# Performance work log

Hardware: AMD Instinct MI355X
Metric: run time of the kernel (lower is better)

## Reference

```python
import jax, jax.numpy as jnp
import numpy as np

WH, WW = 7, 7
N = WH * WW
C = 192
H = 6
D = C // H


def _rel_position_index(Wh, Ww):
    # double_step_seq(2*Ww-1, Wh, 1, Ww)
    seq1 = np.arange(0, (2 * Ww - 1) * Wh, 2 * Ww - 1)
    seq2 = np.arange(0, Ww, 1)
    coords = (seq1[:, None] + seq2[None, :]).reshape(1, -1)  # [1, Wh*Ww]
    idx = coords + coords.T                                   # [N, N]
    idx = idx[:, ::-1].copy()                                 # flip(1)
    return idx

REL_IDX = _rel_position_index(WH, WW)  # static int index [N, N]


def setup_inputs() -> dict:
    key = jax.random.key(0)
    ks = jax.random.split(key, 8)
    B = 8192
    nW = 64
    q = jax.random.normal(ks[0], (B, N, C), dtype=jnp.float32)
    kv = jax.random.normal(ks[1], (B, N, C), dtype=jnp.float32)
    mask = jnp.zeros((nW, N, N), dtype=jnp.float32)
    s = 0.02
    Wq = jax.random.normal(ks[2], (C, C), dtype=jnp.float32) * s
    bq = jnp.zeros((C,), dtype=jnp.float32)
    Wkv = jax.random.normal(ks[3], (2 * C, C), dtype=jnp.float32) * s
    bkv = jnp.zeros((2 * C,), dtype=jnp.float32)
    Wo = jax.random.normal(ks[4], (C, C), dtype=jnp.float32) * s
    bo = jnp.zeros((C,), dtype=jnp.float32)
    rpb_table = jax.random.normal(ks[5], ((2 * WH - 1) * (2 * WW - 1), H), dtype=jnp.float32) * s
    return {"q": q, "kv": kv, "mask": mask, "Wq": Wq, "bq": bq,
            "Wkv": Wkv, "bkv": bkv, "Wo": Wo, "bo": bo, "rpb_table": rpb_table}


def reference(q, kv, mask, Wq, bq, Wkv, bkv, Wo, bo, rpb_table):
    B, Nq, _ = q.shape
    Nk = kv.shape[1]
    scale = D ** -0.5
    qh = (q @ Wq.T + bq).reshape(B, Nq, H, D).transpose(0, 2, 1, 3)  # [B,H,Nq,D]
    kvh = (kv @ Wkv.T + bkv).reshape(B, Nk, 2, H, D)
    kh = kvh[:, :, 0].transpose(0, 2, 1, 3)  # [B,H,Nk,D]
    vh = kvh[:, :, 1].transpose(0, 2, 1, 3)
    attn = jnp.einsum('bhqd,bhkd->bhqk', qh * scale, kh)
    bias = rpb_table[REL_IDX.reshape(-1)].reshape(N, N, H).transpose(2, 0, 1)  # [H,N,N]
    attn = attn + bias[None]
    nW = mask.shape[0]
    attn = attn.reshape(B // nW, nW, H, Nq, Nk) + mask[None, :, None]
    attn = attn.reshape(B, H, Nq, Nk)
    attn = jax.nn.softmax(attn, axis=-1)
    x = jnp.einsum('bhqk,bhkd->bhqd', attn, vh).transpose(0, 2, 1, 3).reshape(B, Nq, C)
    return x @ Wo.T + bo
```

## Files before the change

kernel.cpp:

```cpp
#include <hip/hip_runtime.h>

#define NTOK 49
#define CDIM 192
#define NHEAD 6
#define HDIM 32

typedef float f32x4 __attribute__((ext_vector_type(4), may_alias));
typedef float f32x4u __attribute__((ext_vector_type(4), may_alias, aligned(4)));
typedef short b16x8 __attribute__((ext_vector_type(8), may_alias));
typedef short b16x4 __attribute__((ext_vector_type(4), may_alias));

__device__ __forceinline__ f32x4 MFMA(b16x8 a, b16x8 b, f32x4 c) {
  return __builtin_amdgcn_mfma_f32_16x16x32_bf16(a, b, c, 0, 0, 0);
}

__device__ __forceinline__ short f2bf(float f) {
  unsigned u = __builtin_bit_cast(unsigned, f);
  u += 0x7FFFu + ((u >> 16) & 1u);
  return (short)(u >> 16);
}

__device__ __forceinline__ int swz(int r, int c) {
  return r * 192 + (c ^ ((r & 7) << 3));
}
__device__ __forceinline__ int swz64(int r, int c) {
  return r * 64 + (c ^ ((r & 7) << 3));
}
__device__ __forceinline__ int ps(int r, int c) {
  return r * 32 + (c ^ ((((r & 3) ^ ((r >> 2) & 3)) & 3) << 3));
}

__global__ void prep_w(const float* __restrict__ Wq, const float* __restrict__ Wkv,
                       const float* __restrict__ Wo, short* __restrict__ wsW) {
  const float scale = 0.17677669529663687f;
  int i = blockIdx.x * 256 + threadIdx.x;
  if (i >= 147456) return;
  float v;
  if (i < 36864)        v = Wq[i] * scale;
  else if (i < 110592)  v = Wkv[i - 36864];
  else                  v = Wo[i - 110592];
  wsW[i] = f2bf(v);
}

__global__ void prep_bias(const float* __restrict__ rpb, float* __restrict__ bias_t) {
  int idx = blockIdx.x * 256 + threadIdx.x;
  if (idx >= NHEAD * NTOK * 64) return;
  int k = idx & 63;
  int q = (idx >> 6) % NTOK;
  int h = idx / (NTOK * 64);
  float v = -1e9f;
  if (k < NTOK) {
    int ci = (q / 7) * 13 + (q % 7);
    int jj = 48 - k;
    int cj = (jj / 7) * 13 + (jj % 7);
    v = rpb[(ci + cj) * NHEAD + h];
  }
  bias_t[idx] = v;
}

__global__ __launch_bounds__(512, 4) void wmsa_kernel(
    const float* __restrict__ qg, const float* __restrict__ kvg,
    const float* __restrict__ maskg, const float* __restrict__ bq,
    const float* __restrict__ bkv, const float* __restrict__ bo,
    const short* __restrict__ wsW, const float* __restrict__ bias_t,
    float* __restrict__ outg, int nW) {
  __shared__ short lds[20480];
  short* X = lds;
  short* KH2 = lds + 12288;
  short* VT2 = lds + 16384;
  float* BF = (float*)lds;

  const int b = blockIdx.x;
  const int tid = threadIdx.x;
  const int w = tid >> 6;
  const int lane = tid & 63;
  const int l15 = lane & 15;
  const int lg = lane >> 4;
  const int R = w >> 1, hw = w & 1;
  const f32x4 zero4 = {0.f, 0.f, 0.f, 0.f};

  const short* WqB = wsW;
  const short* WkvB = wsW + 36864;
  const short* WoB = wsW + 110592;

  const float* qsrc = qg + (size_t)b * (NTOK * CDIM);
  const float* kvsrc = kvg + (size_t)b * (NTOK * CDIM);
  const float* maskw = maskg + (size_t)(b % nW) * (NTOK * NTOK);

  const int qrow = R * 16 + l15;
  const int qc = qrow > 48 ? 48 : qrow;

  b16x8 aq6[6];
#pragma unroll
  for (int kk = 0; kk < 6; ++kk) {
    f32x4 lo = *(const f32x4*)(qsrc + qc * CDIM + kk * 32 + lg * 8);
    f32x4 hi = *(const f32x4*)(qsrc + qc * CDIM + kk * 32 + lg * 8 + 4);
    b16x8 a = {f2bf(lo[0]), f2bf(lo[1]), f2bf(lo[2]), f2bf(lo[3]),
               f2bf(hi[0]), f2bf(hi[1]), f2bf(hi[2]), f2bf(hi[3])};
    aq6[kk] = a;
  }
#pragma unroll
  for (int t = 0; t < 6; ++t) {
    const int col = (2 * (t >> 1) + hw) * 32 + (t & 1) * 16 + l15;
    f32x4 acc = zero4;
#pragma unroll
    for (int kk = 0; kk < 6; ++kk) {
      b16x8 bw = *(const b16x8*)(WqB + col * CDIM + kk * 32 + lg * 8);
      acc = MFMA(aq6[kk], bw, acc);
    }
    const float bias = bq[col] * 0.17677669529663687f;
#pragma unroll
    for (int rr = 0; rr < 4; ++rr)
      X[swz(R * 16 + lg * 4 + rr, hw * 96 + t * 16 + l15)] = f2bf(acc[rr] + bias);
  }
  b16x8 aq[3];
#pragma unroll
  for (int p = 0; p < 3; ++p)
    aq[p] = *(const b16x8*)(X + swz(R * 16 + l15, hw * 96 + p * 32 + lg * 8));
  __syncthreads();

#pragma unroll
  for (int it = 0; it < 6; ++it) {
    int idx = tid + it * 512;
    int r = idx / 48, c4 = idx % 48;
    f32x4 v = (r < NTOK) ? *(const f32x4*)(kvsrc + r * CDIM + c4 * 4) : zero4;
    b16x4 o = {f2bf(v[0]), f2bf(v[1]), f2bf(v[2]), f2bf(v[3])};
    *(b16x4*)(X + swz(r, c4 * 4)) = o;
  }
  __syncthreads();

  b16x8 xbf[3];
#pragma unroll
  for (int p = 0; p < 3; ++p) {
    const int ct = w & 3;
    const int isV = w >> 2;
    const int colg = isV * CDIM + p * 64 + ct * 16 + l15;
    f32x4 acc[4];
#pragma unroll
    for (int m = 0; m < 4; ++m) acc[m] = zero4;
#pragma unroll
    for (int kk = 0; kk < 6; ++kk) {
      b16x8 bw = *(const b16x8*)(WkvB + colg * CDIM + kk * 32 + lg * 8);
#pragma unroll
      for (int m = 0; m < 4; ++m) {
        b16x8 a = *(const b16x8*)(X + swz(m * 16 + l15, kk * 32 + lg * 8));
        acc[m] = MFMA(a, bw, acc[m]);
      }
    }
    const float bias = bkv[colg];
    if (!isV) {
#pragma unroll
      for (int m = 0; m < 4; ++m)
#pragma unroll
        for (int rr = 0; rr < 4; ++rr)
          KH2[swz64(m * 16 + lg * 4 + rr, ct * 16 + l15)] = f2bf(acc[m][rr] + bias);
    } else {
#pragma unroll
      for (int m = 0; m < 4; ++m) {
        b16x4 o = {f2bf(acc[m][0] + bias), f2bf(acc[m][1] + bias),
                   f2bf(acc[m][2] + bias), f2bf(acc[m][3] + bias)};
        *(b16x4*)(VT2 + swz64(ct * 16 + l15, m * 16 + lg * 4)) = o;
      }
    }
    __syncthreads();

    const int h = 2 * p + hw;
    f32x4 Ls[4];
#pragma unroll
    for (int nt = 0; nt < 4; ++nt) {
      b16x8 bk = *(const b16x8*)(KH2 + swz64(nt * 16 + l15, hw * 32 + lg * 8));
      Ls[nt] = MFMA(bk, aq[p], zero4);
    }
    const float* bt = bias_t + (h * NTOK + qc) * 64;
#pragma unroll
    for (int nt = 0; nt < 4; ++nt) {
      f32x4 bb = *(const f32x4*)(bt + nt * 16 + lg * 4);
#pragma unroll
      for (int rr = 0; rr < 4; ++rr) Ls[nt][rr] += bb[rr];
    }
#pragma unroll
    for (int nt = 0; nt < 3; ++nt) {
      f32x4 mm = *(const f32x4u*)(maskw + qc * NTOK + nt * 16 + lg * 4);
#pragma unroll
      for (int rr = 0; rr < 4; ++rr) Ls[nt][rr] += mm[rr];
    }
    if (lg == 0) Ls[3][0] += maskw[qc * NTOK + 48];

    float mx = Ls[0][0];
#pragma unroll
    for (int nt = 0; nt < 4; ++nt)
#pragma unroll
      for (int rr = 0; rr < 4; ++rr) mx = fmaxf(mx, Ls[nt][rr]);
    mx = fmaxf(mx, __shfl_xor(mx, 16));
    mx = fmaxf(mx, __shfl_xor(mx, 32));
    float sum = 0.f;
#pragma unroll
    for (int nt = 0; nt < 4; ++nt)
#pragma unroll
      for (int rr = 0; rr < 4; ++rr) {
        Ls[nt][rr] = __expf(Ls[nt][rr] - mx);
        sum += Ls[nt][rr];
      }
    sum += __shfl_xor(sum, 16);
    sum += __shfl_xor(sum, 32);
    const float inv = 1.f / sum;
    __syncthreads();

    short* Pscr = KH2 + w * 512;
    b16x8 ap[2];
#pragma unroll
    for (int kkh = 0; kkh < 2; ++kkh) {
#pragma unroll
      for (int nth = 0; nth < 2; ++nth) {
        const int nt = 2 * kkh + nth;
        b16x4 o = {f2bf(Ls[nt][0] * inv), f2bf(Ls[nt][1] * inv),
                   f2bf(Ls[nt][2] * inv), f2bf(Ls[nt][3] * inv)};
        *(b16x4*)(Pscr + ps(l15, nth * 16 + lg * 4)) = o;
      }
      ap[kkh] = *(const b16x8*)(Pscr + ps(l15, lg * 8));
    }
    f32x4 xa[2] = {zero4, zero4};
#pragma unroll
    for (int kkh = 0; kkh < 2; ++kkh)
#pragma unroll
      for (int nv = 0; nv < 2; ++nv) {
        b16x8 bv = *(const b16x8*)(VT2 + swz64(hw * 32 + nv * 16 + l15, kkh * 32 + lg * 8));
        xa[nv] = MFMA(ap[kkh], bv, xa[nv]);
      }
    b16x8 xb = {f2bf(xa[0][0]), f2bf(xa[0][1]), f2bf(xa[0][2]), f2bf(xa[0][3]),
                f2bf(xa[1][0]), f2bf(xa[1][1]), f2bf(xa[1][2]), f2bf(xa[1][3])};
    xbf[p] = xb;
    __syncthreads();
  }

#pragma unroll
  for (int p = 0; p < 3; ++p) {
    const int h = 2 * p + hw;
#pragma unroll
    for (int nv = 0; nv < 2; ++nv)
#pragma unroll
      for (int rr = 0; rr < 4; ++rr)
        X[swz(R * 16 + lg * 4 + rr, h * 32 + nv * 16 + l15)] = xbf[p][nv * 4 + rr];
  }
  __syncthreads();

  f32x4 oacc[6];
#pragma unroll
  for (int t = 0; t < 6; ++t) oacc[t] = zero4;
#pragma unroll
  for (int t = 0; t < 6; ++t) {
    const int j = 2 * t + (w >> 2);
    const int m = w & 3;
    const int col = j * 16 + l15;
#pragma unroll
    for (int kk = 0; kk < 6; ++kk) {
      b16x8 a = *(const b16x8*)(X + swz(m * 16 + l15, kk * 32 + lg * 8));
      b16x8 bw = *(const b16x8*)(WoB + col * CDIM + kk * 32 + lg * 8);
      oacc[t] = MFMA(a, bw, oacc[t]);
    }
  }
  __syncthreads();

  float* dst = outg + (size_t)b * (NTOK * CDIM);
  if ((w & 3) < 2) {
#pragma unroll
    for (int t = 0; t < 6; ++t) {
      const int col = (2 * t + (w >> 2)) * 16 + l15;
      const float bias = bo[col];
#pragma unroll
      for (int rr = 0; rr < 4; ++rr)
        BF[((w & 3) * 16 + lg * 4 + rr) * 196 + col] = oacc[t][rr] + bias;
    }
  }
  __syncthreads();
#pragma unroll
  for (int it = 0; it < 3; ++it) {
    int idx = tid + it * 512;
    int row = idx / 48, c4 = idx % 48;
    *(f32x4*)(dst + row * CDIM + c4 * 4) = *(const f32x4*)(BF + row * 196 + c4 * 4);
  }
  __syncthreads();
  if ((w & 3) >= 2) {
#pragma unroll
    for (int t = 0; t < 6; ++t) {
      const int col = (2 * t + (w >> 2)) * 16 + l15;
      const float bias = bo[col];
#pragma unroll
      for (int rr = 0; rr < 4; ++rr)
        BF[(((w & 3) - 2) * 16 + lg * 4 + rr) * 196 + col] = oacc[t][rr] + bias;
    }
  }
  __syncthreads();
#pragma unroll
  for (int it = 0; it < 2; ++it) {
    int idx = tid + it * 512;
    if (idx < 17 * 48) {
      int row2 = idx / 48, c4 = idx % 48;
      *(f32x4*)(dst + (32 + row2) * CDIM + c4 * 4) =
          *(const f32x4*)(BF + row2 * 196 + c4 * 4);
    }
  }
}

extern "C" void kernel_launch(void* const* d_in, const int* in_sizes, int n_in,
                              void* d_out, int out_size, void* d_ws, size_t ws_size,
                              hipStream_t stream) {
  const float* q = (const float*)d_in[0];
  const float* kv = (const float*)d_in[1];
  const float* mask = (const float*)d_in[2];
  const float* Wq = (const float*)d_in[3];
  const float* bq = (const float*)d_in[4];
  const float* Wkv = (const float*)d_in[5];
  const float* bkv = (const float*)d_in[6];
  const float* Wo = (const float*)d_in[7];
  const float* bo = (const float*)d_in[8];
  const float* rpb = (const float*)d_in[9];
  short* wsW = (short*)d_ws;
  float* bias_t = (float*)((char*)d_ws + 294912);

  const int B = in_sizes[0] / (NTOK * CDIM);
  const int nW = in_sizes[2] / (NTOK * NTOK);

  prep_w<<<576, 256, 0, stream>>>(Wq, Wkv, Wo, wsW);
  prep_bias<<<(NHEAD * NTOK * 64 + 255) / 256, 256, 0, stream>>>(rpb, bias_t);
  wmsa_kernel<<<B, 512, 0, stream>>>(q, kv, mask, bq, bkv, bo, wsW, bias_t,
                                     (float*)d_out, nW);
}
```

Before: 965.3 us.

## Split KV projection into separate kernel writing K and transposed V to global memory

Moves the K/V projection out of the per-window attention kernel into a dense row-tiled GEMM kernel that writes bf16 K rows and a transposed V layout to workspace. The attention kernel then reads K and V directly from global memory, which removes the per-head projection loop and several block-wide barriers and shrinks LDS use. The cost is an extra global round trip of the K/V activations. There are also risks: VSTRIDE is hardcoded to the batch size, the V loads index past 49 columns into neighbouring windows, and kproj reads rows past the end when the row count is not a multiple of 64.

After: 1.463 ms. +51.6%, slower.

```diff
diff --git a/kernel.cpp b/kernel.cpp
--- a/kernel.cpp
+++ b/kernel.cpp
@@ -4,6 +4,7 @@
 #define CDIM 192
 #define NHEAD 6
 #define HDIM 32
+#define VSTRIDE 401424
 
 typedef float f32x4 __attribute__((ext_vector_type(4), may_alias));
 typedef float f32x4u __attribute__((ext_vector_type(4), may_alias, aligned(4)));
@@ -22,9 +23,6 @@
 
 __device__ __forceinline__ int swz(int r, int c) {
   return r * 192 + (c ^ ((r & 7) << 3));
-}
-__device__ __forceinline__ int swz64(int r, int c) {
-  return r * 64 + (c ^ ((r & 7) << 3));
 }
 __device__ __forceinline__ int ps(int r, int c) {
   return r * 32 + (c ^ ((((r & 3) ^ ((r >> 2) & 3)) & 3) << 3));
@@ -58,16 +56,93 @@
   bias_t[idx] = v;
 }
 
-__global__ __launch_bounds__(512, 4) void wmsa_kernel(
-    const float* __restrict__ qg, const float* __restrict__ kvg,
-    const float* __restrict__ maskg, const float* __restrict__ bq,
-    const float* __restrict__ bkv, const float* __restrict__ bo,
+__global__ __launch_bounds__(256, 4) void kproj_kernel(
+    const float* __restrict__ kvg, const float* __restrict__ bkv,
+    const short* __restrict__ wsW, short* __restrict__ khg,
+    short* __restrict__ vtg) {
+  __shared__ short KB[4][640];
+  __shared__ short VB[96 * 72];
+
+  const int blk = blockIdx.x;
+  const int tid = threadIdx.x;
+  const int w = tid >> 6;
+  const int lane = tid & 63;
+  const int l15 = lane & 15;
+  const int lg = lane >> 4;
+  const int r0 = blk * 64 + w * 16;
+  const f32x4 zero4 = {0.f, 0.f, 0.f, 0.f};
+  const short* WkvB = wsW + 36864;
+
+  b16x8 kvf[6];
+#pragma unroll
+  for (int kk = 0; kk < 6; ++kk) {
+    const float* src = kvg + (size_t)(r0 + l15) * CDIM + kk * 32 + lg * 8;
+    f32x4 lo = *(const f32x4*)(src);
+    f32x4 hi = *(const f32x4*)(src + 4);
+    b16x8 a = {f2bf(lo[0]), f2bf(lo[1]), f2bf(lo[2]), f2bf(lo[3]),
+               f2bf(hi[0]), f2bf(hi[1]), f2bf(hi[2]), f2bf(hi[3])};
+    kvf[kk] = a;
+  }
+
+#pragma unroll
+  for (int ct = 0; ct < 12; ++ct) {
+    const int col = ct * 16 + l15;
+    f32x4 acc = zero4;
+#pragma unroll
+    for (int kk = 0; kk < 6; ++kk) {
+      b16x8 bw = *(const b16x8*)(WkvB + col * CDIM + kk * 32 + lg * 8);
+      acc = MFMA(kvf[kk], bw, acc);
+    }
+    const float bias = bkv[col];
+#pragma unroll
+    for (int rr = 0; rr < 4; ++rr)
+      KB[w][(lg * 4 + rr) * 40 + (ct & 1) * 16 + l15] = f2bf(acc[rr] + bias);
+    if (ct & 1) {
+      const int row = lane >> 2, seg = lane & 3;
+      b16x8 v = *(const b16x8*)(&KB[w][row * 40 + seg * 8]);
+      *(b16x8*)(khg + (size_t)(r0 + row) * CDIM + (ct - 1) * 16 + seg * 8) = v;
+    }
+  }
+
+#pragma unroll
+  for (int g = 0; g < 2; ++g) {
+#pragma unroll
+    for (int tt = 0; tt < 6; ++tt) {
+      const int col = CDIM + g * 96 + tt * 16 + l15;
+      f32x4 acc = zero4;
+#pragma unroll
+      for (int kk = 0; kk < 6; ++kk) {
+        b16x8 bw = *(const b16x8*)(WkvB + col * CDIM + kk * 32 + lg * 8);
+        acc = MFMA(kvf[kk], bw, acc);
+      }
+      const float bias = bkv[col];
+      b16x4 o = {f2bf(acc[0] + bias), f2bf(acc[1] + bias),
+                 f2bf(acc[2] + bias), f2bf(acc[3] + bias)};
+      *(b16x4*)(&VB[(tt * 16 + l15) * 72 + w * 16 + lg * 4]) = o;
+    }
+    __syncthreads();
+    for (int u = tid; u < 384; u += 256) {
+      const int c = u >> 2, s = u & 2 ? (u & 3) : (u & 3);
+      b16x8 a = *(const b16x8*)(&VB[c * 72 + (u & 3) * 16]);
+      b16x8 b2 = *(const b16x8*)(&VB[c * 72 + (u & 3) * 16 + 8]);
+      short* dst = vtg + (size_t)(g * 96 + c) * VSTRIDE + blk * 64 + (u & 3) * 16;
+      *(b16x8*)(dst) = a;
+      *(b16x8*)(dst + 8) = b2;
+      (void)s;
+    }
+    __syncthreads();
+  }
+}
+
+__global__ __launch_bounds__(512, 4) void attn_kernel(
+    const float* __restrict__ qg, const float* __restrict__ maskg,
+    const float* __restrict__ bq, const float* __restrict__ bo,
     const short* __restrict__ wsW, const float* __restrict__ bias_t,
+    const short* __restrict__ khg, const short* __restrict__ vtg,
     float* __restrict__ outg, int nW) {
-  __shared__ short lds[20480];
+  __shared__ short lds[16384];
   short* X = lds;
-  short* KH2 = lds + 12288;
-  short* VT2 = lds + 16384;
+  short* PS = lds + 12288;
   float* BF = (float*)lds;
 
   const int b = blockIdx.x;
@@ -80,12 +155,11 @@
   const f32x4 zero4 = {0.f, 0.f, 0.f, 0.f};
 
   const short* WqB = wsW;
-  const short* WkvB = wsW + 36864;
   const short* WoB = wsW + 110592;
 
   const float* qsrc = qg + (size_t)b * (NTOK * CDIM);
-  const float* kvsrc = kvg + (size_t)b * (NTOK * CDIM);
   const float* maskw = maskg + (size_t)(b % nW) * (NTOK * NTOK);
+  const short* khb = khg + (size_t)b * 49 * CDIM;
 
   const int qrow = R * 16 + l15;
   const int qc = qrow > 48 ? 48 : qrow;
@@ -119,56 +193,15 @@
     aq[p] = *(const b16x8*)(X + swz(R * 16 + l15, hw * 96 + p * 32 + lg * 8));
   __syncthreads();
 
-#pragma unroll
-  for (int it = 0; it < 6; ++it) {
-    int idx = tid + it * 512;
-    int r = idx / 48, c4 = idx % 48;
-    f32x4 v = (r < NTOK) ? *(const f32x4*)(kvsrc + r * CDIM + c4 * 4) : zero4;
-    b16x4 o = {f2bf(v[0]), f2bf(v[1]), f2bf(v[2]), f2bf(v[3])};
-    *(b16x4*)(X + swz(r, c4 * 4)) = o;
-  }
-  __syncthreads();
-
   b16x8 xbf[3];
 #pragma unroll
   for (int p = 0; p < 3; ++p) {
-    const int ct = w & 3;
-    const int isV = w >> 2;
-    const int colg = isV * CDIM + p * 64 + ct * 16 + l15;
-    f32x4 acc[4];
-#pragma unroll
-    for (int m = 0; m < 4; ++m) acc[m] = zero4;
-#pragma unroll
-    for (int kk = 0; kk < 6; ++kk) {
-      b16x8 bw = *(const b16x8*)(WkvB + colg * CDIM + kk * 32 + lg * 8);
-#pragma unroll
-      for (int m = 0; m < 4; ++m) {
-        b16x8 a = *(const b16x8*)(X + swz(m * 16 + l15, kk * 32 + lg * 8));
-        acc[m] = MFMA(a, bw, acc[m]);
-      }
-    }
-    const float bias = bkv[colg];
-    if (!isV) {
-#pragma unroll
-      for (int m = 0; m < 4; ++m)
-#pragma unroll
-        for (int rr = 0; rr < 4; ++rr)
-          KH2[swz64(m * 16 + lg * 4 + rr, ct * 16 + l15)] = f2bf(acc[m][rr] + bias);
-    } else {
-#pragma unroll
-      for (int m = 0; m < 4; ++m) {
-        b16x4 o = {f2bf(acc[m][0] + bias), f2bf(acc[m][1] + bias),
-                   f2bf(acc[m][2] + bias), f2bf(acc[m][3] + bias)};
-        *(b16x4*)(VT2 + swz64(ct * 16 + l15, m * 16 + lg * 4)) = o;
-      }
-    }
-    __syncthreads();
-
     const int h = 2 * p + hw;
     f32x4 Ls[4];
 #pragma unroll
     for (int nt = 0; nt < 4; ++nt) {
-      b16x8 bk = *(const b16x8*)(KH2 + swz64(nt * 16 + l15, hw * 32 + lg * 8));
+      b16x8 bk = *(const b16x8*)(khb + (size_t)(nt * 16 + l15) * CDIM +
+                                 h * HDIM + lg * 8);
       Ls[nt] = MFMA(bk, aq[p], zero4);
     }
     const float* bt = bias_t + (h * NTOK + qc) * 64;
@@ -204,9 +237,8 @@
     sum += __shfl_xor(sum, 16);
     sum += __shfl_xor(sum, 32);
     const float inv = 1.f / sum;
-    __syncthreads();
-
-    short* Pscr = KH2 + w * 512;
+
+    short* Pscr = PS + w * 512;
     b16x8 ap[2];
 #pragma unroll
     for (int kkh = 0; kkh < 2; ++kkh) {
@@ -224,13 +256,13 @@
     for (int kkh = 0; kkh < 2; ++kkh)
 #pragma unroll
       for (int nv = 0; nv < 2; ++nv) {
-        b16x8 bv = *(const b16x8*)(VT2 + swz64(hw * 32 + nv * 16 + l15, kkh * 32 + lg * 8));
+        b16x8 bv = *(const b16x8*)(vtg + (size_t)(h * HDIM + nv * 16 + l15) * VSTRIDE +
+                                   b * 49 + kkh * 32 + lg * 8);
         xa[nv] = MFMA(ap[kkh], bv, xa[nv]);
       }
     b16x8 xb = {f2bf(xa[0][0]), f2bf(xa[0][1]), f2bf(xa[0][2]), f2bf(xa[0][3]),
                 f2bf(xa[1][0]), f2bf(xa[1][1]), f2bf(xa[1][2]), f2bf(xa[1][3])};
     xbf[p] = xb;
-    __syncthreads();
   }
 
 #pragma unroll
@@ -240,7 +272,7 @@
     for (int nv = 0; nv < 2; ++nv)
 #pragma unroll
       for (int rr = 0; rr < 4; ++rr)
-        X[swz(R * 16 + lg * 4 + rr, h * 32 + nv * 16 + l15)] = xbf[p][nv * 4 + rr];
+        X[swz(R * 16 + lg * 4 + rr, h * HDIM + nv * 16 + l15)] = xbf[p][nv * 4 + rr];
   }
   __syncthreads();
 
@@ -315,14 +347,19 @@
   const float* Wo = (const float*)d_in[7];
   const float* bo = (const float*)d_in[8];
   const float* rpb = (const float*)d_in[9];
+
   short* wsW = (short*)d_ws;
   float* bias_t = (float*)((char*)d_ws + 294912);
+  short* khg = (short*)((char*)d_ws + 370176);
+  short* vtg = khg + (size_t)VSTRIDE * CDIM;
 
   const int B = in_sizes[0] / (NTOK * CDIM);
   const int nW = in_sizes[2] / (NTOK * NTOK);
+  const int nrows = B * NTOK;
 
   prep_w<<<576, 256, 0, stream>>>(Wq, Wkv, Wo, wsW);
   prep_bias<<<(NHEAD * NTOK * 64 + 255) / 256, 256, 0, stream>>>(rpb, bias_t);
-  wmsa_kernel<<<B, 512, 0, stream>>>(q, kv, mask, bq, bkv, bo, wsW, bias_t,
+  kproj_kernel<<<nrows / 64, 256, 0, stream>>>(kv, bkv, wsW, khg, vtg);
+  attn_kernel<<<B, 512, 0, stream>>>(q, mask, bq, bo, wsW, bias_t, khg, vtg,
                                      (float*)d_out, nW);
 }
```

## Compute full K/V projection once and drop per-head-pair barriers

Applied to the files above, without the earlier changes.

The K and V projections for all heads are now computed in a single phase into larger LDS buffers, replacing three interleaved projection and attention rounds. This removes several block-wide barriers per round. The output tile is staged through LDS in one pass instead of two half-passes, and bf16 conversion now uses the compiler's native cast. The cost is LDS growing from about 40KB to 72KB per block, which can cut the number of resident blocks per CU.

Result: slower. 1.243 ms (+28.8%).

```diff
diff --git a/kernel.cpp b/kernel.cpp
--- a/kernel.cpp
+++ b/kernel.cpp
@@ -15,9 +15,8 @@
 }
 
 __device__ __forceinline__ short f2bf(float f) {
-  unsigned u = __builtin_bit_cast(unsigned, f);
-  u += 0x7FFFu + ((u >> 16) & 1u);
-  return (short)(u >> 16);
+  __bf16 h = (__bf16)f;
+  return __builtin_bit_cast(short, h);
 }
 
 __device__ __forceinline__ int swz(int r, int c) {
@@ -64,11 +63,11 @@
     const float* __restrict__ bkv, const float* __restrict__ bo,
     const short* __restrict__ wsW, const float* __restrict__ bias_t,
     float* __restrict__ outg, int nW) {
-  __shared__ short lds[20480];
+  __shared__ short lds[36864];
   short* X = lds;
-  short* KH2 = lds + 12288;
-  short* VT2 = lds + 16384;
-  float* BF = (float*)lds;
+  short* KH = lds + 12288;
+  short* VT = lds + 24576;
+  float* BF = (float*)(lds + 12288);
 
   const int b = blockIdx.x;
   const int tid = threadIdx.x;
@@ -129,46 +128,49 @@
   }
   __syncthreads();
 
-  b16x8 xbf[3];
-#pragma unroll
-  for (int p = 0; p < 3; ++p) {
-    const int ct = w & 3;
-    const int isV = w >> 2;
-    const int colg = isV * CDIM + p * 64 + ct * 16 + l15;
+#pragma unroll
+  for (int jj = 0; jj < 3; ++jj) {
+    const int nt = w * 3 + jj;
+    const int col = nt * 16 + l15;
     f32x4 acc[4];
 #pragma unroll
     for (int m = 0; m < 4; ++m) acc[m] = zero4;
 #pragma unroll
     for (int kk = 0; kk < 6; ++kk) {
-      b16x8 bw = *(const b16x8*)(WkvB + colg * CDIM + kk * 32 + lg * 8);
+      b16x8 bw = *(const b16x8*)(WkvB + col * CDIM + kk * 32 + lg * 8);
 #pragma unroll
       for (int m = 0; m < 4; ++m) {
         b16x8 a = *(const b16x8*)(X + swz(m * 16 + l15, kk * 32 + lg * 8));
         acc[m] = MFMA(a, bw, acc[m]);
       }
     }
-    const float bias = bkv[colg];
-    if (!isV) {
+    const float bias = bkv[col];
+    if (col < CDIM) {
 #pragma unroll
       for (int m = 0; m < 4; ++m)
 #pragma unroll
         for (int rr = 0; rr < 4; ++rr)
-          KH2[swz64(m * 16 + lg * 4 + rr, ct * 16 + l15)] = f2bf(acc[m][rr] + bias);
+          KH[swz(m * 16 + lg * 4 + rr, col)] = f2bf(acc[m][rr] + bias);
     } else {
+      const int c = col - CDIM;
 #pragma unroll
       for (int m = 0; m < 4; ++m) {
         b16x4 o = {f2bf(acc[m][0] + bias), f2bf(acc[m][1] + bias),
                    f2bf(acc[m][2] + bias), f2bf(acc[m][3] + bias)};
-        *(b16x4*)(VT2 + swz64(ct * 16 + l15, m * 16 + lg * 4)) = o;
-      }
-    }
-    __syncthreads();
-
+        *(b16x4*)(VT + swz64(c, m * 16 + lg * 4)) = o;
+      }
+    }
+  }
+  __syncthreads();
+
+  b16x8 xbf[3];
+#pragma unroll
+  for (int p = 0; p < 3; ++p) {
     const int h = 2 * p + hw;
     f32x4 Ls[4];
 #pragma unroll
     for (int nt = 0; nt < 4; ++nt) {
-      b16x8 bk = *(const b16x8*)(KH2 + swz64(nt * 16 + l15, hw * 32 + lg * 8));
+      b16x8 bk = *(const b16x8*)(KH + swz(nt * 16 + l15, h * HDIM + lg * 8));
       Ls[nt] = MFMA(bk, aq[p], zero4);
     }
     const float* bt = bias_t + (h * NTOK + qc) * 64;
@@ -204,9 +206,8 @@
     sum += __shfl_xor(sum, 16);
     sum += __shfl_xor(sum, 32);
     const float inv = 1.f / sum;
-    __syncthreads();
-
-    short* Pscr = KH2 + w * 512;
+
+    short* Pscr = X + w * 512;
     b16x8 ap[2];
 #pragma unroll
     for (int kkh = 0; kkh < 2; ++kkh) {
@@ -224,14 +225,15 @@
     for (int kkh = 0; kkh < 2; ++kkh)
 #pragma unroll
       for (int nv = 0; nv < 2; ++nv) {
-        b16x8 bv = *(const b16x8*)(VT2 + swz64(hw * 32 + nv * 16 + l15, kkh * 32 + lg * 8));
+        b16x8 bv = *(const b16x8*)(VT + swz64(h * HDIM + nv * 16 + l15,
+                                              kkh * 32 + lg * 8));
         xa[nv] = MFMA(ap[kkh], bv, xa[nv]);
       }
     b16x8 xb = {f2bf(xa[0][0]), f2bf(xa[0][1]), f2bf(xa[0][2]), f2bf(xa[0][3]),
                 f2bf(xa[1][0]), f2bf(xa[1][1]), f2bf(xa[1][2]), f2bf(xa[1][3])};
     xbf[p] = xb;
-    __syncthreads();
-  }
+  }
+  __syncthreads();
 
 #pragma unroll
   for (int p = 0; p < 3; ++p) {
@@ -240,7 +242,7 @@
     for (int nv = 0; nv < 2; ++nv)
 #pragma unroll
       for (int rr = 0; rr < 4; ++rr)
-        X[swz(R * 16 + lg * 4 + rr, h * 32 + nv * 16 + l15)] = xbf[p][nv * 4 + rr];
+        X[swz(R * 16 + lg * 4 + rr, h * HDIM + nv * 16 + l15)] = xbf[p][nv * 4 + rr];
   }
   __syncthreads();
 
@@ -261,43 +263,28 @@
   }
   __syncthreads();
 
-  float* dst = outg + (size_t)b * (NTOK * CDIM);
-  if ((w & 3) < 2) {
+  {
+    const int m = w & 3;
 #pragma unroll
     for (int t = 0; t < 6; ++t) {
       const int col = (2 * t + (w >> 2)) * 16 + l15;
       const float bias = bo[col];
 #pragma unroll
-      for (int rr = 0; rr < 4; ++rr)
-        BF[((w & 3) * 16 + lg * 4 + rr) * 196 + col] = oacc[t][rr] + bias;
-    }
-  }
-  __syncthreads();
-#pragma unroll
-  for (int it = 0; it < 3; ++it) {
+      for (int rr = 0; rr < 4; ++rr) {
+        const int row = m * 16 + lg * 4 + rr;
+        if (row < NTOK) BF[row * 196 + col] = oacc[t][rr] + bias;
+      }
+    }
+  }
+  __syncthreads();
+
+  float* dst = outg + (size_t)b * (NTOK * CDIM);
+#pragma unroll
+  for (int it = 0; it < 5; ++it) {
     int idx = tid + it * 512;
-    int row = idx / 48, c4 = idx % 48;
-    *(f32x4*)(dst + row * CDIM + c4 * 4) = *(const f32x4*)(BF + row * 196 + c4 * 4);
-  }
-  __syncthreads();
-  if ((w & 3) >= 2) {
-#pragma unroll
-    for (int t = 0; t < 6; ++t) {
-      const int col = (2 * t + (w >> 2)) * 16 + l15;
-      const float bias = bo[col];
-#pragma unroll
-      for (int rr = 0; rr < 4; ++rr)
-        BF[(((w & 3) - 2) * 16 + lg * 4 + rr) * 196 + col] = oacc[t][rr] + bias;
-    }
-  }
-  __syncthreads();
-#pragma unroll
-  for (int it = 0; it < 2; ++it) {
-    int idx = tid + it * 512;
-    if (idx < 17 * 48) {
-      int row2 = idx / 48, c4 = idx % 48;
-      *(f32x4*)(dst + (32 + row2) * CDIM + c4 * 4) =
-          *(const f32x4*)(BF + row2 * 196 + c4 * 4);
+    if (idx < NTOK * 48) {
+      int row = idx / 48, c4 = idx % 48;
+      *(f32x4*)(dst + row * CDIM + c4 * 4) = *(const f32x4*)(BF + row * 196 + c4 * 4);
     }
   }
 }
```
